# Performance work log

Measured on AMD Instinct MI355X. Metric: run time of the kernel, lower is better.

The kernel has to match this reference:

```python
import jax, jax.numpy as jnp
import numpy as np

HEAD_DIM = 128
N_HEADS = 32
NEG_INF = -1e9


def apply_rope(x, cos, sin):
    # x: (B, S, H, D); cos/sin: (S, D//2). Pairs (x[...,2i], x[...,2i+1]) form
    # complex numbers (torch.view_as_complex on reshape(..., -1, 2)).
    xr = x[..., 0::2]
    xi = x[..., 1::2]
    c = cos[None, :, None, :]
    s = sin[None, :, None, :]
    out_r = xr * c - xi * s
    out_i = xr * s + xi * c
    return jnp.stack([out_r, out_i], axis=-1).reshape(x.shape)


def setup_inputs() -> dict:
    key = jax.random.key(0)
    ks = jax.random.split(key, 8)
    B, S, D = 2, 1024, 4096
    hd = HEAD_DIM
    x = jax.random.normal(ks[0], (B, S, D), dtype=jnp.float32)
    # true RoPE frequencies
    theta = 10000.0 ** (-np.arange(0, hd, 2, dtype=np.float32) / hd)  # (hd/2,)
    angles = np.arange(S, dtype=np.float32)[:, None] * theta[None, :]  # (S, hd/2)
    freqs_cos = jnp.asarray(np.cos(angles))
    freqs_sin = jnp.asarray(np.sin(angles))
    # causal additive mask
    mask = jnp.where(jnp.triu(jnp.ones((S, S), dtype=bool), k=1), NEG_INF, 0.0)
    mask = mask[None, None, :, :].astype(jnp.float32)
    scale = 0.02
    wq = jax.random.normal(ks[1], (D, D), dtype=jnp.float32) * scale
    wk = jax.random.normal(ks[2], (D, D), dtype=jnp.float32) * scale
    wv = jax.random.normal(ks[3], (D, D), dtype=jnp.float32) * scale
    wo = jax.random.normal(ks[4], (D, D), dtype=jnp.float32) * scale
    cache_k = jnp.zeros((B, S, N_HEADS, hd), dtype=jnp.float32)
    cache_v = jnp.zeros((B, S, N_HEADS, hd), dtype=jnp.float32)
    return {
        "x": x, "start_pos": 0, "freqs_cos": freqs_cos, "freqs_sin": freqs_sin,
        "mask": mask, "cache_k": cache_k, "cache_v": cache_v,
        "wq": wq, "wk": wk, "wv": wv, "wo": wo,
    }


def reference(x, start_pos, freqs_cos, freqs_sin, mask, cache_k, cache_v, wq, wk, wv, wo):
    B, S, D = x.shape
    H, hd = N_HEADS, HEAD_DIM
    # QKV projections (torch Linear: y = x @ W.T)
    xq = jnp.einsum('bsd,od->bso', x, wq).reshape(B, S, H, hd)
    xk = jnp.einsum('bsd,od->bso', x, wk).reshape(B, S, H, hd)
    xv = jnp.einsum('bsd,od->bso', x, wv).reshape(B, S, H, hd)
    xq = apply_rope(xq, freqs_cos, freqs_sin)
    xk = apply_rope(xk, freqs_cos, freqs_sin)
    # KV-cache append (n_rep == 1, so repeat_kv is identity)
    cache_k = jax.lax.dynamic_update_slice(cache_k, xk, (0, start_pos, 0, 0))
    cache_v = jax.lax.dynamic_update_slice(cache_v, xv, (0, start_pos, 0, 0))
    kv_len = start_pos + S
    keys = cache_k[:, :kv_len]
    values = cache_v[:, :kv_len]
    # attention: energy -> mask -> scaled softmax -> weighted sum
    energy = jnp.einsum('bqhd,bkhd->bhqk', xq, keys)
    energy = energy + mask
    scores = jax.nn.softmax(energy.astype(jnp.float32) / jnp.sqrt(jnp.float32(hd)), axis=-1).astype(xq.dtype)
    out = jnp.einsum('bhqk,bkhd->bqhd', scores, values).reshape(B, S, H * hd)
    return jnp.einsum('bso,do->bsd', out, wo)
```

## Files before the change

kernel.cpp:

```cpp
#include <hip/hip_runtime.h>
#include <hip/hip_bf16.h>
#include <stdint.h>
#include <stddef.h>

typedef __bf16 bf16_t;
typedef __attribute__((ext_vector_type(8))) __bf16 bf16x8;
typedef __attribute__((ext_vector_type(4))) float f32x4;
typedef __attribute__((ext_vector_type(16))) float f32x16;
typedef __attribute__((ext_vector_type(4))) uint32_t u32x4;

#define D_MODEL 4096
#define SEQ 1024
#define NH 32
#define HD 128
#define MTOT 2048

#define VMCNT(n) asm volatile("s_waitcnt vmcnt(" #n ")" ::: "memory")
#define LGKM0() asm volatile("s_waitcnt lgkmcnt(0)" ::: "memory")
#define SCHED0() __builtin_amdgcn_sched_barrier(0)

__device__ __forceinline__ void gload_lds16(const void* g, void* l) {
  __builtin_amdgcn_global_load_lds((const __attribute__((address_space(1))) uint32_t*)g,
                                   (__attribute__((address_space(3))) uint32_t*)l, 16, 0, 0);
}

__device__ __forceinline__ uint32_t cvtpk(float lo, float hi) {
  uint32_t r;
  asm("v_cvt_pk_bf16_f32 %0, %1, %2" : "=v"(r) : "v"(lo), "v"(hi));
  return r;
}
__device__ __forceinline__ void plswap(uint32_t& a, uint32_t& b) {
  asm volatile("v_permlane32_swap_b32 %0, %1" : "+v"(a), "+v"(b));
}

__global__ void dtype_probe(const uint32_t* __restrict__ x, uint32_t* __restrict__ flag) {
  const int lane = threadIdx.x & 63;
  const uint32_t w = x[lane];
  const uint32_t e = (w >> 7) & 0xFF;
  const bool inband = (e >= 100 && e <= 140);
  const unsigned long long m = __ballot(inband);
  if (lane == 0) *flag = (__popcll(m) >= 32) ? 1u : 0u;
}

__global__ __launch_bounds__(256) void conv_bf16(const void* __restrict__ src,
                                                 bf16_t* __restrict__ dst, int n,
                                                 const uint32_t* __restrict__ flag) {
  const int i = (blockIdx.x * 256 + threadIdx.x) * 8;
  if (i >= n) return;
  if (*flag) {
    *(bf16x8*)(dst + i) = *(const bf16x8*)((const bf16_t*)src + i);
  } else {
    const float4 a = *(const float4*)((const float*)src + i);
    const float4 b = *(const float4*)((const float*)src + i + 4);
    bf16x8 v;
    v[0] = (bf16_t)a.x; v[1] = (bf16_t)a.y; v[2] = (bf16_t)a.z; v[3] = (bf16_t)a.w;
    v[4] = (bf16_t)b.x; v[5] = (bf16_t)b.y; v[6] = (bf16_t)b.z; v[7] = (bf16_t)b.w;
    *(bf16x8*)(dst + i) = v;
  }
}

template <int MODE>
__global__ __launch_bounds__(512, 2) void gemm_bt(
    const bf16_t* __restrict__ A, const bf16_t* __restrict__ B,
    void* __restrict__ dstv, const uint32_t* __restrict__ flagp,
    const bf16_t* __restrict__ fcos, const bf16_t* __restrict__ fsin) {
  __shared__ __align__(16) char smem[3 * 49152];
  const int tid = threadIdx.x;
  const int lane = tid & 63, wid = tid >> 6;
  const int fr = lane & 15, fq = lane >> 4;
  const int wm = wid >> 2, wn = wid & 3;
  const int d = (int)(blockIdx.x + gridDim.x * blockIdx.y);
  const int st = ((d & 7) << 1) | ((d >> 3) & 1);
  const int ist = d >> 4;
  const int bxs = (st & 3) * 4 + (ist & 3);
  const int bys = (st >> 2) * 4 + (ist >> 2);
  const int bm0 = bxs * 128, bn0 = bys * 256;
  const bool isbf = (MODE == 2) ? (*flagp != 0) : true;

  auto stage_half = [&](int t, int bi, int h) {
    const int k0 = t * 64;
    char* ab = smem + bi * 49152;
    char* bb = ab + 16384;
    {
      const int o = h * 8192 + tid * 16;
      const int row = o >> 7, ch = (o >> 4) & 7;
      gload_lds16(A + (size_t)(bm0 + row) * D_MODEL + k0 + ((ch ^ (row & 7)) * 8), ab + o);
    }
#pragma unroll
    for (int j = 0; j < 2; ++j) {
      const int o = (h * 2 + j) * 8192 + tid * 16;
      const int row = o >> 7, ch = (o >> 4) & 7;
      gload_lds16(B + (size_t)(bn0 + row) * D_MODEL + k0 + ((ch ^ (row & 7)) * 8), bb + o);
    }
  };

  f32x4 acc[4][4];
#pragma unroll
  for (int m = 0; m < 4; m++)
#pragma unroll
    for (int n = 0; n < 4; n++) acc[m][n] = f32x4{0.f, 0.f, 0.f, 0.f};

  auto phase_nb = [&](int bi, int kk) {
    const char* ab = smem + bi * 49152;
    const char* bb = ab + 16384;
    const int swz = ((kk * 4 + fq) ^ (fr & 7)) << 4;
    bf16x8 af[4], bfv[4];
#pragma unroll
    for (int m = 0; m < 4; ++m)
      af[m] = *(const bf16x8*)(ab + (wm * 64 + m * 16 + fr) * 128 + swz);
#pragma unroll
    for (int n = 0; n < 4; ++n)
      bfv[n] = *(const bf16x8*)(bb + (wn * 64 + n * 16 + fr) * 128 + swz);
    __builtin_amdgcn_s_setprio(1);
#pragma unroll
    for (int m = 0; m < 4; ++m)
#pragma unroll
      for (int n = 0; n < 4; ++n)
        acc[m][n] = __builtin_amdgcn_mfma_f32_16x16x32_bf16(af[m], bfv[n], acc[m][n], 0, 0, 0);
    __builtin_amdgcn_s_setprio(0);
  };

  const int NT = D_MODEL / 64;
  stage_half(0, 0, 0); stage_half(0, 0, 1);
  stage_half(1, 1, 0); stage_half(1, 1, 1);
  VMCNT(6);
  __builtin_amdgcn_s_barrier();
  int cur = 0, nxt = 2;
  for (int t = 0; t < NT - 2; ++t) {
    stage_half(t + 2, nxt, 0);
    stage_half(t + 2, nxt, 1);
    phase_nb(cur, 0);
    phase_nb(cur, 1);
    VMCNT(6);
    __builtin_amdgcn_s_barrier();
    cur = (cur == 2) ? 0 : cur + 1;
    nxt = (nxt == 2) ? 0 : nxt + 1;
  }
  phase_nb(cur, 0);
  phase_nb(cur, 1);
  VMCNT(0);
  __builtin_amdgcn_s_barrier();
  cur = (cur == 2) ? 0 : cur + 1;
  phase_nb(cur, 0);
  phase_nb(cur, 1);

#pragma unroll
  for (int m = 0; m < 4; m++) {
#pragma unroll
    for (int n = 0; n < 4; n++) {
      const int gn = bn0 + wn * 64 + n * 16 + fr;
#pragma unroll
      for (int r = 0; r < 4; r++) {
        const int gm = bm0 + wm * 64 + m * 16 + fq * 4 + r;
        const float vv = acc[m][n][r];
        if constexpr (MODE == 0) {
          const float pv = __shfl_xor(vv, 1);
          const int s = gm & (SEQ - 1);
          const int i = (gn & (HD - 1)) >> 1;
          const float c = (float)fcos[s * 64 + i];
          const float si = (float)fsin[s * 64 + i];
          const float outv = (gn & 1) ? (pv * si + vv * c) : (vv * c - pv * si);
          const int b = gm >> 10, h = gn >> 7, dd = gn & (HD - 1);
          ((bf16_t*)dstv)[((size_t)(b * NH + h) * SEQ + s) * HD + dd] = (bf16_t)outv;
        } else if constexpr (MODE == 1) {
          const int b = gm >> 10, s = gm & (SEQ - 1), h = gn >> 7, dd = gn & (HD - 1);
          ((bf16_t*)dstv)[((size_t)(b * NH + h) * HD + dd) * SEQ + s] = (bf16_t)vv;
        } else {
          if (isbf) ((bf16_t*)dstv)[(size_t)gm * D_MODEL + gn] = (bf16_t)vv;
          else      ((float*)dstv)[(size_t)gm * D_MODEL + gn] = vv;
        }
      }
    }
  }
}

__global__ __launch_bounds__(512, 2) void attn_fwd(
    const bf16_t* __restrict__ Q, const bf16_t* __restrict__ K,
    const bf16_t* __restrict__ V, bf16_t* __restrict__ Out) {
  constexpr float SC = 0.088388347648318447f;
  constexpr float MNEG = -10000.0f;
  __shared__ __align__(16) char smem[65536];
  const int tid = threadIdx.x, lane = tid & 63, wid = tid >> 6;
  const int l31 = lane & 31, hi = lane >> 5, l7 = lane & 7;
  const int qt = 3 - (int)blockIdx.x;
  const int bh = blockIdx.y;
  const int qb0 = qt * 256;
  const int q0w = qb0 + wid * 32;
  const int nt = qt * 4 + 4;

  const bf16_t* Kbase = K + (size_t)bh * SEQ * HD;
  const bf16_t* Vbase = V + (size_t)bh * HD * SEQ;

  bf16x8 qa[8];
  {
    const bf16_t* qp = Q + ((size_t)bh * SEQ + q0w + l31) * HD + hi * 8;
#pragma unroll
    for (int ks = 0; ks < 8; ++ks) qa[ks] = *(const bf16x8*)(qp + ks * 16);
  }

  auto stage = [&](int t, int bi) {
    const int kv0 = t * 64;
#pragma unroll
    for (int pass = 0; pass < 2; ++pass) {
      const int o = pass * 8192 + tid * 16;
      {
        const int row = o >> 8, ch = (o & 255) >> 4;
        gload_lds16(Kbase + (size_t)(kv0 + row) * HD + ((ch ^ (row & 7)) * 8),
                    smem + bi * 16384 + o);
      }
      {
        const int row = o >> 7, ch = (o & 127) >> 4;
        gload_lds16(Vbase + (size_t)row * SEQ + kv0 + ((ch ^ (row & 7)) * 8),
                    smem + 32768 + bi * 16384 + o);
      }
    }
  };

  f32x16 Oacc[4];
#pragma unroll
  for (int i = 0; i < 4; ++i)
#pragma unroll
    for (int j = 0; j < 16; ++j) Oacc[i][j] = 0.f;
  float mrow = MNEG, lrow = 0.f;

  stage(0, 0);
  stage(1, 1);
  VMCNT(4);
  __builtin_amdgcn_s_barrier();

  for (int t = 0; t < nt; ++t) {
    const int kv0 = t * 64;
    if (kv0 < q0w + 32) {
      const char* kb_ = smem + (t & 1) * 16384;
      const char* vb_ = smem + 32768 + (t & 1) * 16384;

      f32x16 sacc[2];
#pragma unroll
      for (int kb = 0; kb < 2; ++kb)
#pragma unroll
        for (int j = 0; j < 16; ++j) sacc[kb][j] = 0.f;
      __builtin_amdgcn_s_setprio(1);
#pragma unroll
      for (int kb = 0; kb < 2; ++kb)
#pragma unroll
        for (int ks = 0; ks < 8; ++ks) {
          bf16x8 kf = *(const bf16x8*)(kb_ + (kb * 32 + l31) * 256 +
                                       (((ks * 2 + hi) ^ l7) << 4));
          sacc[kb] = __builtin_amdgcn_mfma_f32_32x32x16_bf16(kf, qa[ks], sacc[kb], 0, 0, 0);
        }
      __builtin_amdgcn_s_setprio(0);

      const bool diag = (kv0 + 63 > q0w);
      float pm = MNEG;
#pragma unroll
      for (int kb = 0; kb < 2; ++kb)
#pragma unroll
        for (int r = 0; r < 16; ++r) {
          float x = sacc[kb][r] * SC;
          if (diag) {
            const int kvpos = kv0 + kb * 32 + (r & 3) + 8 * (r >> 2) + 4 * hi;
            if (kvpos > q0w + l31) x = MNEG;
          }
          sacc[kb][r] = x;
          pm = fmaxf(pm, x);
        }
      pm = fmaxf(pm, __shfl_xor(pm, 32));
      const float mn = fmaxf(mrow, pm);
      const float al = __expf(mrow - mn);
      mrow = mn;
      float ps = 0.f;
#pragma unroll
      for (int kb = 0; kb < 2; ++kb)
#pragma unroll
        for (int r = 0; r < 16; ++r) {
          const float e = __expf(sacc[kb][r] - mn);
          sacc[kb][r] = e;
          ps += e;
        }
      lrow = lrow * al + ps;
#pragma unroll
      for (int db = 0; db < 4; ++db)
#pragma unroll
        for (int j = 0; j < 16; ++j) Oacc[db][j] *= al;

      uint32_t pw[16];
#pragma unroll
      for (int kb = 0; kb < 2; ++kb) {
        const int o8 = kb * 8;
        pw[o8 + 0] = cvtpk(sacc[kb][0], sacc[kb][1]);
        pw[o8 + 1] = cvtpk(sacc[kb][2], sacc[kb][3]);
        pw[o8 + 2] = cvtpk(sacc[kb][4], sacc[kb][5]);
        pw[o8 + 3] = cvtpk(sacc[kb][6], sacc[kb][7]);
        plswap(pw[o8 + 0], pw[o8 + 2]);
        plswap(pw[o8 + 1], pw[o8 + 3]);
        pw[o8 + 4] = cvtpk(sacc[kb][8], sacc[kb][9]);
        pw[o8 + 5] = cvtpk(sacc[kb][10], sacc[kb][11]);
        pw[o8 + 6] = cvtpk(sacc[kb][12], sacc[kb][13]);
        pw[o8 + 7] = cvtpk(sacc[kb][14], sacc[kb][15]);
        plswap(pw[o8 + 4], pw[o8 + 6]);
        plswap(pw[o8 + 5], pw[o8 + 7]);
      }

      __builtin_amdgcn_s_setprio(1);
#pragma unroll
      for (int db = 0; db < 4; ++db)
#pragma unroll
        for (int ks2 = 0; ks2 < 4; ++ks2) {
          bf16x8 vf = *(const bf16x8*)(vb_ + (db * 32 + l31) * 128 +
                                       (((ks2 * 2 + hi) ^ l7) << 4));
          union { u32x4 u; bf16x8 v; } pc;
          pc.u = u32x4{pw[ks2 * 4], pw[ks2 * 4 + 1], pw[ks2 * 4 + 2], pw[ks2 * 4 + 3]};
          Oacc[db] = __builtin_amdgcn_mfma_f32_32x32x16_bf16(vf, pc.v, Oacc[db], 0, 0, 0);
        }
      __builtin_amdgcn_s_setprio(0);
    }

    __builtin_amdgcn_s_barrier();
    if (t + 2 < nt) {
      stage(t + 2, t & 1);
      VMCNT(4);
    } else if (t + 1 < nt) {
      VMCNT(0);
    }
    __builtin_amdgcn_s_barrier();
  }

  lrow += __shfl_xor(lrow, 32);
  const float linv = 1.0f / fmaxf(lrow, 1e-20f);

  {
    char* ob = smem + wid * 8192;
#pragma unroll
    for (int db = 0; db < 4; ++db)
#pragma unroll
      for (int rp = 0; rp < 8; ++rp) {
        const int r = rp * 2;
        const int d = db * 32 + (r & 3) + 8 * (r >> 2) + 4 * hi;
        const uint32_t w = cvtpk(Oacc[db][r] * linv, Oacc[db][r + 1] * linv);
        *(uint32_t*)(ob + l31 * 256 + ((d * 2) ^ ((l31 & 7) << 4))) = w;
      }
  }
  __builtin_amdgcn_s_barrier();
  const int b = bh >> 5, h = bh & 31;
#pragma unroll
  for (int pass = 0; pass < 8; ++pass) {
    const int o = pass * 8192 + tid * 16;
    const int row = o >> 8, ch = (o & 255) >> 4;
    const u32x4 val = *(const u32x4*)(smem + row * 256 + ((ch ^ (row & 7)) << 4));
    *(u32x4*)(Out + ((size_t)(b * SEQ + qb0 + row)) * D_MODEL + h * HD + ch * 8) = val;
  }
}

extern "C" void kernel_launch(void* const* d_in, const int* in_sizes, int n_in,
                              void* d_out, int out_size, void* d_ws, size_t ws_size,
                              hipStream_t stream) {
  (void)in_sizes; (void)n_in; (void)out_size;
  const void* x_raw    = d_in[0];
  const void* fcos_raw = d_in[2];
  const void* fsin_raw = d_in[3];
  const void* wq_raw   = d_in[7];
  const void* wk_raw   = d_in[8];
  const void* wv_raw   = d_in[9];
  const void* wo_raw   = d_in[10];

  const size_t NX = (size_t)MTOT * D_MODEL;
  const size_t NW = (size_t)D_MODEL * D_MODEL;
  const size_t NF = SEQ * (HD / 2);

  char* base = (char*)d_ws;
  uint32_t* flag = (uint32_t*)base;
  bf16_t* fc = (bf16_t*)(base + 4096);
  bf16_t* fs = (bf16_t*)(base + 4096 + 131072);
  bf16_t* elems = (bf16_t*)(base + (1 << 20));
  bf16_t* xc = elems;
  bf16_t* w0 = xc + NX;
  bf16_t* w1 = w0 + NW;
  bf16_t* q_ws = w1 + NW;
  bf16_t* k_ws = q_ws + NX;
  bf16_t* v_ws = k_ws + NX;
  bf16_t* a_ws = v_ws + NX;
  const size_t NEED = (1 << 20) + 2 * (5 * NX + 2 * NW);
  if (ws_size < NEED) return;

  dtype_probe<<<1, 64, 0, stream>>>((const uint32_t*)x_raw, flag);

  const int cb_x = (int)(NX / (256 * 8));
  const int cb_w = (int)(NW / (256 * 8));
  const int cb_f = (int)(NF / (256 * 8));
  conv_bf16<<<cb_x, 256, 0, stream>>>(x_raw, xc, (int)NX, flag);
  conv_bf16<<<cb_f, 256, 0, stream>>>(fcos_raw, fc, (int)NF, flag);
  conv_bf16<<<cb_f, 256, 0, stream>>>(fsin_raw, fs, (int)NF, flag);

  dim3 gg(MTOT / 128, D_MODEL / 256);
  conv_bf16<<<cb_w, 256, 0, stream>>>(wq_raw, w0, (int)NW, flag);
  gemm_bt<0><<<gg, 512, 0, stream>>>(xc, w0, q_ws, flag, fc, fs);
  conv_bf16<<<cb_w, 256, 0, stream>>>(wk_raw, w1, (int)NW, flag);
  gemm_bt<0><<<gg, 512, 0, stream>>>(xc, w1, k_ws, flag, fc, fs);
  conv_bf16<<<cb_w, 256, 0, stream>>>(wv_raw, w0, (int)NW, flag);
  gemm_bt<1><<<gg, 512, 0, stream>>>(xc, w0, v_ws, flag, fc, fs);

  attn_fwd<<<dim3(4, 2 * NH), 512, 0, stream>>>(q_ws, k_ws, v_ws, a_ws);

  conv_bf16<<<cb_w, 256, 0, stream>>>(wo_raw, w1, (int)NW, flag);
  gemm_bt<2><<<gg, 512, 0, stream>>>(a_ws, w1, d_out, flag, fc, fs);
}
```

Before: 399.7 us.

## Restructure projection GEMM to 4 waves with 64x128 warp tiles and BK=32

The projection GEMM goes from 8 waves to 4 waves per block. Each wave now computes a 64x128 sub-tile (32 accumulators) instead of 64x64, and the K step shrinks from 64 to 32 with a matching 64-byte-row LDS swizzle. This cuts LDS footprint and raises per-wave register reuse of A/B fragments. In exchange, barrier iterations double, each wave needs more accumulator registers (risking spills or lower occupancy), and fewer waves are available to hide latency. The VMCNT(6) wait still matches the six loads issued per stage.

```diff
diff --git a/kernel.cpp b/kernel.cpp
--- a/kernel.cpp
+++ b/kernel.cpp
@@ -60,15 +60,15 @@
 }
 
 template <int MODE>
-__global__ __launch_bounds__(512, 2) void gemm_bt(
+__global__ __launch_bounds__(256, 2) void gemm_bt(
     const bf16_t* __restrict__ A, const bf16_t* __restrict__ B,
     void* __restrict__ dstv, const uint32_t* __restrict__ flagp,
     const bf16_t* __restrict__ fcos, const bf16_t* __restrict__ fsin) {
-  __shared__ __align__(16) char smem[3 * 49152];
+  __shared__ __align__(16) char smem[3 * 24576];
   const int tid = threadIdx.x;
   const int lane = tid & 63, wid = tid >> 6;
   const int fr = lane & 15, fq = lane >> 4;
-  const int wm = wid >> 2, wn = wid & 3;
+  const int wm = wid >> 1, wn = wid & 1;
   const int d = (int)(blockIdx.x + gridDim.x * blockIdx.y);
   const int st = ((d & 7) << 1) | ((d >> 3) & 1);
   const int ist = d >> 4;
@@ -77,78 +77,75 @@
   const int bm0 = bxs * 128, bn0 = bys * 256;
   const bool isbf = (MODE == 2) ? (*flagp != 0) : true;
 
-  auto stage_half = [&](int t, int bi, int h) {
-    const int k0 = t * 64;
-    char* ab = smem + bi * 49152;
-    char* bb = ab + 16384;
-    {
-      const int o = h * 8192 + tid * 16;
-      const int row = o >> 7, ch = (o >> 4) & 7;
-      gload_lds16(A + (size_t)(bm0 + row) * D_MODEL + k0 + ((ch ^ (row & 7)) * 8), ab + o);
-    }
-#pragma unroll
-    for (int j = 0; j < 2; ++j) {
-      const int o = (h * 2 + j) * 8192 + tid * 16;
-      const int row = o >> 7, ch = (o >> 4) & 7;
-      gload_lds16(B + (size_t)(bn0 + row) * D_MODEL + k0 + ((ch ^ (row & 7)) * 8), bb + o);
+  auto stage = [&](int t, int bi) {
+    const int k0 = t * 32;
+    char* ab = smem + bi * 24576;
+    char* bb = ab + 8192;
+#pragma unroll
+    for (int p = 0; p < 2; ++p) {
+      const int o = p * 4096 + tid * 16;
+      const int row = o >> 6, ch = (o >> 4) & 3;
+      gload_lds16(A + (size_t)(bm0 + row) * D_MODEL + k0 + ((ch ^ ((row >> 1) & 3)) * 8), ab + o);
+    }
+#pragma unroll
+    for (int p = 0; p < 4; ++p) {
+      const int o = p * 4096 + tid * 16;
+      const int row = o >> 6, ch = (o >> 4) & 3;
+      gload_lds16(B + (size_t)(bn0 + row) * D_MODEL + k0 + ((ch ^ ((row >> 1) & 3)) * 8), bb + o);
     }
   };
 
-  f32x4 acc[4][4];
+  f32x4 acc[4][8];
 #pragma unroll
   for (int m = 0; m < 4; m++)
 #pragma unroll
-    for (int n = 0; n < 4; n++) acc[m][n] = f32x4{0.f, 0.f, 0.f, 0.f};
-
-  auto phase_nb = [&](int bi, int kk) {
-    const char* ab = smem + bi * 49152;
-    const char* bb = ab + 16384;
-    const int swz = ((kk * 4 + fq) ^ (fr & 7)) << 4;
-    bf16x8 af[4], bfv[4];
+    for (int n = 0; n < 8; n++) acc[m][n] = f32x4{0.f, 0.f, 0.f, 0.f};
+
+  auto compute = [&](int bi) {
+    const char* ab = smem + bi * 24576;
+    const char* bb = ab + 8192;
+    const int swz = (fq ^ ((fr >> 1) & 3)) << 4;
+    bf16x8 af[4], bfv[8];
 #pragma unroll
     for (int m = 0; m < 4; ++m)
-      af[m] = *(const bf16x8*)(ab + (wm * 64 + m * 16 + fr) * 128 + swz);
-#pragma unroll
-    for (int n = 0; n < 4; ++n)
-      bfv[n] = *(const bf16x8*)(bb + (wn * 64 + n * 16 + fr) * 128 + swz);
+      af[m] = *(const bf16x8*)(ab + (wm * 64 + m * 16 + fr) * 64 + swz);
+#pragma unroll
+    for (int n = 0; n < 8; ++n)
+      bfv[n] = *(const bf16x8*)(bb + (wn * 128 + n * 16 + fr) * 64 + swz);
     __builtin_amdgcn_s_setprio(1);
 #pragma unroll
     for (int m = 0; m < 4; ++m)
 #pragma unroll
-      for (int n = 0; n < 4; ++n)
+      for (int n = 0; n < 8; ++n)
         acc[m][n] = __builtin_amdgcn_mfma_f32_16x16x32_bf16(af[m], bfv[n], acc[m][n], 0, 0, 0);
     __builtin_amdgcn_s_setprio(0);
   };
 
-  const int NT = D_MODEL / 64;
-  stage_half(0, 0, 0); stage_half(0, 0, 1);
-  stage_half(1, 1, 0); stage_half(1, 1, 1);
+  const int NT = D_MODEL / 32;
+  stage(0, 0);
+  stage(1, 1);
   VMCNT(6);
   __builtin_amdgcn_s_barrier();
   int cur = 0, nxt = 2;
   for (int t = 0; t < NT - 2; ++t) {
-    stage_half(t + 2, nxt, 0);
-    stage_half(t + 2, nxt, 1);
-    phase_nb(cur, 0);
-    phase_nb(cur, 1);
+    stage(t + 2, nxt);
+    compute(cur);
     VMCNT(6);
     __builtin_amdgcn_s_barrier();
     cur = (cur == 2) ? 0 : cur + 1;
     nxt = (nxt == 2) ? 0 : nxt + 1;
   }
-  phase_nb(cur, 0);
-  phase_nb(cur, 1);
+  compute(cur);
   VMCNT(0);
   __builtin_amdgcn_s_barrier();
   cur = (cur == 2) ? 0 : cur + 1;
-  phase_nb(cur, 0);
-  phase_nb(cur, 1);
+  compute(cur);
 
 #pragma unroll
   for (int m = 0; m < 4; m++) {
 #pragma unroll
-    for (int n = 0; n < 4; n++) {
-      const int gn = bn0 + wn * 64 + n * 16 + fr;
+    for (int n = 0; n < 8; n++) {
+      const int gn = bn0 + wn * 128 + n * 16 + fr;
 #pragma unroll
       for (int r = 0; r < 4; r++) {
         const int gm = bm0 + wm * 64 + m * 16 + fq * 4 + r;
@@ -393,14 +390,14 @@
 
   dim3 gg(MTOT / 128, D_MODEL / 256);
   conv_bf16<<<cb_w, 256, 0, stream>>>(wq_raw, w0, (int)NW, flag);
-  gemm_bt<0><<<gg, 512, 0, stream>>>(xc, w0, q_ws, flag, fc, fs);
+  gemm_bt<0><<<gg, 256, 0, stream>>>(xc, w0, q_ws, flag, fc, fs);
   conv_bf16<<<cb_w, 256, 0, stream>>>(wk_raw, w1, (int)NW, flag);
-  gemm_bt<0><<<gg, 512, 0, stream>>>(xc, w1, k_ws, flag, fc, fs);
+  gemm_bt<0><<<gg, 256, 0, stream>>>(xc, w1, k_ws, flag, fc, fs);
   conv_bf16<<<cb_w, 256, 0, stream>>>(wv_raw, w0, (int)NW, flag);
-  gemm_bt<1><<<gg, 512, 0, stream>>>(xc, w0, v_ws, flag, fc, fs);
+  gemm_bt<1><<<gg, 256, 0, stream>>>(xc, w0, v_ws, flag, fc, fs);
 
   attn_fwd<<<dim3(4, 2 * NH), 512, 0, stream>>>(q_ws, k_ws, v_ws, a_ws);
 
   conv_bf16<<<cb_w, 256, 0, stream>>>(wo_raw, w1, (int)NW, flag);
-  gemm_bt<2><<<gg, 512, 0, stream>>>(a_ws, w1, d_out, flag, fc, fs);
-}
+  gemm_bt<2><<<gg, 256, 0, stream>>>(a_ws, w1, d_out, flag, fc, fs);
+}
```

New measurement: 435.0 us. 8.8% more time.
